# Kernel tuning notes

Hardware: AMD Instinct MI355X
Metric: run time of the kernel (lower is better)

## Reference

```python
import jax, jax.numpy as jnp
import numpy as np

B, C, H, W = 4, 512, 64, 64
CQ = C // 8


def setup_inputs() -> dict:
    key = jax.random.key(0)
    ks = jax.random.split(key, 8)
    s_in = 1.0 / np.sqrt(C)
    return {
        "x": jax.random.normal(ks[0], (B, C, H, W), jnp.float32),
        "wq": jax.random.normal(ks[1], (CQ, C), jnp.float32) * s_in,
        "bq": jax.random.normal(ks[2], (CQ,), jnp.float32) * 0.01,
        "wk": jax.random.normal(ks[3], (CQ, C), jnp.float32) * s_in,
        "bk": jax.random.normal(ks[4], (CQ,), jnp.float32) * 0.01,
        "wv": jax.random.normal(ks[5], (C, C), jnp.float32) * s_in,
        "bv": jax.random.normal(ks[6], (C,), jnp.float32) * 0.01,
        "gamma": jax.random.normal(ks[7], (1,), jnp.float32) * 0.1,
    }


def reference(x, wq, bq, wk, bk, wv, bv, gamma):
    b, c, h, w = x.shape
    n = h * w
    xf = x.reshape(b, c, n)  # [B, C, N]; 1x1 conv == channel matmul
    q = jnp.einsum("oc,bcn->bon", wq, xf) + bq[None, :, None]  # [B, CQ, N]
    k = jnp.einsum("oc,bcn->bon", wk, xf) + bk[None, :, None]  # [B, CQ, N]
    v = jnp.einsum("oc,bcn->bon", wv, xf) + bv[None, :, None]  # [B, C, N]
    energy = jnp.einsum("bcn,bcm->bnm", q, k)  # [B, N, N]
    attn = jax.nn.softmax(energy, axis=-1)
    out = jnp.einsum("bcm,bnm->bcn", v, attn)  # [B, C, N]
    out = out.reshape(b, c, h, w)
    return gamma[0] * out + x
```

## Files before the change

kernel.cpp:

```cpp
#include <hip/hip_runtime.h>
#include <hip/hip_bf16.h>

#define BATCH 4
#define CH    512
#define NPIX  4096
#define LOG2E 1.4426950408889634f

#define BOFF  327680
#define WTOT  328320
#define PSTR  268

typedef float v4f __attribute__((ext_vector_type(4)));
typedef short v8s __attribute__((ext_vector_type(8)));
typedef unsigned short u16;

__device__ __forceinline__ float b2f(u16 v){
    union { unsigned u; float f; } x; x.u = ((unsigned)v) << 16; return x.f;
}
__device__ __forceinline__ u16 f2b(float f){
    union { float f; unsigned u; } x; x.f = f;
    unsigned r = x.u + 0x7fffu + ((x.u >> 16) & 1u);
    return (u16)(r >> 16);
}
__device__ __forceinline__ void f2b2(float a, float b, u16* o){
    union { __hip_bfloat162 v; u16 s[2]; } u;
    u.v = __float22bfloat162_rn(make_float2(a, b));
    o[0] = u.s[0]; o[1] = u.s[1];
}
__device__ __forceinline__ float fexp2(float x){
#if __has_builtin(__builtin_amdgcn_exp2f)
    return __builtin_amdgcn_exp2f(x);
#else
    return exp2f(x);
#endif
}
__device__ __forceinline__ v4f mfma16(v8s a, v8s b, v4f c){
    return __builtin_amdgcn_mfma_f32_16x16x32_bf16(a, b, c, 0, 0, 0);
}
__device__ __forceinline__ float load_s(const void* p, size_t idx, int isf32){
    return isf32 ? ((const float*)p)[idx] : b2f(((const u16*)p)[idx]);
}

__device__ __forceinline__ int sniff_isf32(const unsigned* __restrict__ xw,
                                           int t, int nthr, int* cnt){
    if (t == 0) *cnt = 0;
    __syncthreads();
    int c = 0;
    for (int i = t; i < 1024; i += nthr){
        unsigned e = (xw[i] >> 23) & 0xFFu;
        if (e >= 64u && e < 192u) c++;
    }
    c += __shfl_xor(c, 1);  c += __shfl_xor(c, 2);  c += __shfl_xor(c, 4);
    c += __shfl_xor(c, 8);  c += __shfl_xor(c, 16); c += __shfl_xor(c, 32);
    if ((t & 63) == 0) atomicAdd(cnt, c);
    __syncthreads();
    return (*cnt > 512) ? 1 : 0;
}

__global__ __launch_bounds__(256) void prep_kernel(
    const void* __restrict__ wq, const void* __restrict__ bq,
    const void* __restrict__ wk, const void* __restrict__ bk,
    const void* __restrict__ wv, const void* __restrict__ bv,
    const void* __restrict__ x, u16* __restrict__ wall)
{
    __shared__ int scnt;
    const int isf32 = sniff_isf32((const unsigned*)x, threadIdx.x, 256, &scnt);

    int i = blockIdx.x * 256 + threadIdx.x;
    if (i >= WTOT) return;
    float v;
    if (i < BOFF){
        int o = i >> 9, c = i & 511;
        if (o < 64)       v = load_s(wq, (size_t)o * 512 + c, isf32);
        else if (o < 128) v = load_s(wk, (size_t)(o - 64) * 512 + c, isf32);
        else              v = load_s(wv, (size_t)(o - 128) * 512 + c, isf32);
    } else {
        int o = i - BOFF;
        if (o < 64)       v = load_s(bq, o, isf32);
        else if (o < 128) v = load_s(bk, o - 64, isf32);
        else              v = load_s(bv, o - 128, isf32);
    }
    wall[i] = f2b(v);
}

__global__ __launch_bounds__(256, 3) void proj_kernel(
    const void* __restrict__ x, const u16* __restrict__ wall,
    u16* __restrict__ Qf, u16* __restrict__ Kf, u16* __restrict__ Vf,
    u16* __restrict__ xbf)
{
    __shared__ __align__(16) u16 xT[2][64 * 40];
    __shared__ int scnt;

    const int isf32 = sniff_isf32((const unsigned*)x, threadIdx.x, 256, &scnt);

    const int ntile = blockIdx.x, os = blockIdx.y, b = blockIdx.z;
    const int n0 = ntile * 64;
    const int t = threadIdx.x, lane = t & 63, w = t >> 6, q = lane >> 4, col = lane & 15;

    const int rrow  = t >> 3;
    const int ncol8 = (t & 7) * 8;
    const int xswz  = (t & 3) << 3;
    const size_t xbase = (size_t)b * CH * NPIX + n0 + ncol8;

    v4f acc[5][4];
    #pragma unroll
    for (int i = 0; i < 5; i++)
        #pragma unroll
        for (int j = 0; j < 4; j++) acc[i][j] = (v4f){0.f, 0.f, 0.f, 0.f};

    float4 gn0, gn1;

    #define LOADX(cb_) do {                                                  \
        const size_t src = xbase + (size_t)((cb_) * 32 + rrow) * NPIX;       \
        if (isf32){ gn0 = *(const float4*)((const float*)x + src);           \
                    gn1 = *(const float4*)((const float*)x + src + 4); }     \
        else { union { uint4 v; float4 f; } lu;                              \
               lu.v = *(const uint4*)((const u16*)x + src); gn0 = lu.f; }    \
    } while (0)

    #define CVT8(vals_) do {                                                 \
        if (isf32){ f2b2(gn0.x, gn0.y, &vals_[0]); f2b2(gn0.z, gn0.w, &vals_[2]); \
                    f2b2(gn1.x, gn1.y, &vals_[4]); f2b2(gn1.z, gn1.w, &vals_[6]); } \
        else { union { float4 f; uint4 v; } uu; uu.f = gn0;                  \
               *(uint4*)vals_ = uu.v; }                                      \
    } while (0)

    {
        LOADX(0);
        u16 vals[8]; CVT8(vals);
        #pragma unroll
        for (int i = 0; i < 8; i++) xT[0][(ncol8 + i) * 40 + (rrow ^ xswz)] = vals[i];
        if (os == 0)
            *(uint4*)&xbf[(size_t)(b * CH + rrow) * NPIX + n0 + ncol8] = *(uint4*)vals;
        LOADX(1);
    }
    __syncthreads();

    for (int cb = 0; cb < 16; cb++){
        const int buf = cb & 1;
        const int c0 = cb * 32 + q * 8;

        v8s wf[5];
        #pragma unroll
        for (int ct = 0; ct < 5; ct++)
            wf[ct] = *(const v8s*)&wall[(size_t)(320 * os + 80 * w + 16 * ct + col) * 512 + c0];

        v8s a[4];
        #pragma unroll
        for (int g = 0; g < 4; g++){
            const int rsw = ((2 * g + (col >> 3)) & 3) << 3;
            a[g] = *(const v8s*)&xT[buf][(16 * g + col) * 40 + (rsw ^ (q * 8))];
        }

        if (cb < 15){
            u16 vals[8]; CVT8(vals);
            #pragma unroll
            for (int i = 0; i < 8; i++) xT[buf ^ 1][(ncol8 + i) * 40 + (rrow ^ xswz)] = vals[i];
            if (os == 0)
                *(uint4*)&xbf[(size_t)(b * CH + (cb + 1) * 32 + rrow) * NPIX + n0 + ncol8] = *(uint4*)vals;
            if (cb < 14) LOADX(cb + 2);
        }

        #pragma unroll
        for (int ct = 0; ct < 5; ct++)
            #pragma unroll
            for (int g = 0; g < 4; g++)
                acc[ct][g] = mfma16(a[g], wf[ct], acc[ct][g]);
        __syncthreads();
    }
    #undef LOADX
    #undef CVT8

    const u16* ball = wall + BOFF;
    #pragma unroll
    for (int ct = 0; ct < 5; ct++){
        const int o = 320 * os + 80 * w + 16 * ct + col;
        const float bv_ = b2f(ball[o]);
        #pragma unroll
        for (int g = 0; g < 4; g++){
            const int nb = n0 + 16 * g + 4 * q;
            if (o < 64){
                const int k = o;
                size_t base = (size_t)b * NPIX * 64
                    + ((size_t)((nb >> 4) * 2 + (k >> 5))) * 512
                    + ((k & 31) >> 3) * 128 + (nb & 15) * 8 + (k & 7);
                #pragma unroll
                for (int r = 0; r < 4; r++)
                    Qf[base + r * 8] = f2b((acc[ct][g][r] + bv_) * LOG2E);
            } else if (o < 128){
                const int k = o - 64;
                size_t base = (size_t)b * NPIX * 64
                    + ((size_t)((nb >> 4) * 2 + (k >> 5))) * 512
                    + ((k & 31) >> 3) * 128 + (nb & 15) * 8 + (k & 7);
                #pragma unroll
                for (int r = 0; r < 4; r++)
                    Kf[base + r * 8] = f2b(acc[ct][g][r] + bv_);
            } else {
                const int c = o - 128;
                size_t base = (size_t)b * CH * NPIX
                    + ((size_t)((c >> 4) * 128 + (nb >> 5))) * 512
                    + ((nb & 31) >> 3) * 128 + (c & 15) * 8 + (nb & 7);
                union { uint2 u; u16 s[4]; } ov;
                #pragma unroll
                for (int r = 0; r < 4; r++)
                    ov.s[r] = f2b(acc[ct][g][r] + bv_);
                *(uint2*)&Vf[base] = ov.u;
            }
        }
    }
}

__global__ __launch_bounds__(512, 4) void attn_kernel(
    const void* __restrict__ x,
    const u16* __restrict__ Qf, const u16* __restrict__ Kf, const u16* __restrict__ Vf,
    const u16* __restrict__ xbf, const void* __restrict__ gamma,
    void* __restrict__ out)
{
    __shared__ __align__(16) u16  Plds[2][64 * PSTR];
    __shared__ __align__(16) float lsum[8][64];
    __shared__ int scnt;

    const int isf32 = sniff_isf32((const unsigned*)x, threadIdx.x, 512, &scnt);

    const int bid = blockIdx.x;
    const int csplit = bid & 1;
    const int b      = (bid >> 1) & 3;
    const int ntile  = bid >> 3;
    const int n0 = ntile * 64;

    const int t = threadIdx.x, lane = t & 63, w = t >> 6, q = lane >> 4, col = lane & 15;

    const u16* Qb = Qf + (size_t)b * NPIX * 64;
    const u16* Kb = Kf + (size_t)b * NPIX * 64;
    const u16* Vb = Vf + (size_t)b * CH * NPIX;

    v8s qa[4][2];
    #pragma unroll
    for (int g = 0; g < 4; g++)
        #pragma unroll
        for (int c2 = 0; c2 < 2; c2++)
            qa[g][c2] = *(const v8s*)&Qb[(size_t)(((n0 >> 4) + g) * 2 + c2) * 512 + lane * 8];

    float lreg[4] = {0.f, 0.f, 0.f, 0.f};

    v4f oacc[2][4];
    #pragma unroll
    for (int i = 0; i < 2; i++)
        #pragma unroll
        for (int j = 0; j < 4; j++) oacc[i][j] = (v4f){0.f, 0.f, 0.f, 0.f};

    const int ms    = 32 * w;
    const int cslab = csplit * 256 + 32 * w;

    for (int it = 0; it < 16; it++){
        const int m0 = it * 256;
        const int buf = it & 1;

        v8s kf[2][2];
        #pragma unroll
        for (int mt = 0; mt < 2; mt++)
            #pragma unroll
            for (int c2 = 0; c2 < 2; c2++)
                kf[mt][c2] = *(const v8s*)&Kb[(size_t)((((m0 + ms) >> 4) + mt) * 2 + c2) * 512 + lane * 8];

        #pragma unroll
        for (int g = 0; g < 4; g++){
            #pragma unroll
            for (int mt = 0; mt < 2; mt++){
                v4f sv = (v4f){-64.f, -64.f, -64.f, -64.f};
                sv = mfma16(kf[mt][0], qa[g][0], sv);
                sv = mfma16(kf[mt][1], qa[g][1], sv);
                float p0 = fexp2(sv[0]), p1 = fexp2(sv[1]);
                float p2 = fexp2(sv[2]), p3 = fexp2(sv[3]);
                lreg[g] += (p0 + p1) + (p2 + p3);
                union { uint2 u; u16 s[4]; } pk;
                f2b2(p0, p1, &pk.s[0]);
                f2b2(p2, p3, &pk.s[2]);
                *(uint2*)&Plds[buf][(16 * g + col) * PSTR + ms + 16 * mt + 4 * q] = pk.u;
            }
        }

        __syncthreads();

        v8s va_c[2];
        #pragma unroll
        for (int ct = 0; ct < 2; ct++)
            va_c[ct] = *(const v8s*)&Vb[(size_t)(((cslab + 16 * ct) >> 4) * 128 + (m0 >> 5)) * 512 + lane * 8];
        #pragma unroll
        for (int kk = 0; kk < 8; kk++){
            v8s va_n[2];
            if (kk < 7){
                #pragma unroll
                for (int ct = 0; ct < 2; ct++)
                    va_n[ct] = *(const v8s*)&Vb[(size_t)(((cslab + 16 * ct) >> 4) * 128 + (m0 >> 5) + kk + 1) * 512 + lane * 8];
            }
            v8s pb[4];
            #pragma unroll
            for (int nt = 0; nt < 4; nt++)
                pb[nt] = *(const v8s*)&Plds[buf][(16 * nt + col) * PSTR + 32 * kk + q * 8];
            __builtin_amdgcn_s_setprio(1);
            #pragma unroll
            for (int ct = 0; ct < 2; ct++)
                #pragma unroll
                for (int nt = 0; nt < 4; nt++)
                    oacc[ct][nt] = mfma16(va_c[ct], pb[nt], oacc[ct][nt]);
            __builtin_amdgcn_s_setprio(0);
            #pragma unroll
            for (int ct = 0; ct < 2; ct++) va_c[ct] = va_n[ct];
        }
    }

    #pragma unroll
    for (int g = 0; g < 4; g++){
        lreg[g] += __shfl_xor(lreg[g], 16);
        lreg[g] += __shfl_xor(lreg[g], 32);
    }
    if (lane < 16){
        #pragma unroll
        for (int g = 0; g < 4; g++)
            lsum[w][16 * g + lane] = lreg[g];
    }
    __syncthreads();

    const float gam = load_s(gamma, 0, isf32);
    float linv[4];
    #pragma unroll
    for (int nt = 0; nt < 4; nt++){
        int nn = 16 * nt + col;
        float l = ((lsum[0][nn] + lsum[1][nn]) + (lsum[2][nn] + lsum[3][nn]))
                + ((lsum[4][nn] + lsum[5][nn]) + (lsum[6][nn] + lsum[7][nn]));
        linv[nt] = gam / l;
    }

    const size_t boff = (size_t)b * CH * NPIX;
    #pragma unroll
    for (int ct = 0; ct < 2; ct++){
        #pragma unroll
        for (int rr = 0; rr < 4; rr++){
            int c = cslab + 16 * ct + 4 * q + rr;
            size_t base = boff + (size_t)c * NPIX + n0;
            #pragma unroll
            for (int nt = 0; nt < 4; nt++){
                int n = 16 * nt + col;
                float o = oacc[ct][nt][rr] * linv[nt] + b2f(xbf[base + n]);
                if (isf32) ((float*)out)[base + n] = o;
                else       ((u16*)out)[base + n]  = f2b(o);
            }
        }
    }
}

extern "C" void kernel_launch(void* const* d_in, const int* in_sizes, int n_in,
                              void* d_out, int out_size, void* d_ws, size_t ws_size,
                              hipStream_t stream)
{
    const void* x     = d_in[0];
    const void* wq    = d_in[1];
    const void* bq    = d_in[2];
    const void* wk    = d_in[3];
    const void* bk    = d_in[4];
    const void* wv    = d_in[5];
    const void* bv    = d_in[6];
    const void* gamma = d_in[7];

    u16* Qf   = (u16*)d_ws;
    u16* Kf   = Qf + (size_t)1048576;
    u16* Vf   = Kf + (size_t)1048576;
    u16* xbf  = Vf + (size_t)8388608;
    u16* wall = xbf + (size_t)8388608;

    prep_kernel<<<(WTOT + 255) / 256, 256, 0, stream>>>(wq, bq, wk, bk, wv, bv, x, wall);
    proj_kernel<<<dim3(64, 2, BATCH), 256, 0, stream>>>(x, wall, Qf, Kf, Vf, xbf);
    attn_kernel<<<512, 512, 0, stream>>>(x, Qf, Kf, Vf, xbf, gamma, d_out);
}
```

Measured before the change: 207.6 us.

## Stage two channel blocks per barrier and pre-tile weights for coalesced fragment loads

The projection kernel now processes two 32-channel blocks per iteration. LDS tiles are doubled and two global x loads are kept in flight, which halves the number of __syncthreads. The prep kernel writes the weight matrix in a tiled order so each warp's MFMA B-fragments for a block are contiguous 512-element chunks, replacing strided row reads. Occupancy hint drops from 3 to 2 blocks per CU to make room for the extra registers and LDS.

```diff
diff --git a/kernel.cpp b/kernel.cpp
--- a/kernel.cpp
+++ b/kernel.cpp
@@ -74,21 +74,27 @@
         if (o < 64)       v = load_s(wq, (size_t)o * 512 + c, isf32);
         else if (o < 128) v = load_s(wk, (size_t)(o - 64) * 512 + c, isf32);
         else              v = load_s(wv, (size_t)(o - 128) * 512 + c, isf32);
+        const int os = o / 320, rem = o % 320;
+        const int w = rem / 80, ct = (rem % 80) / 16, col = rem % 16;
+        const int cb = c >> 5, q = (c >> 3) & 3, e = c & 7;
+        const size_t idx = (size_t)(((os * 4 + w) * 5 + ct) * 16 + cb) * 512
+                         + col * 32 + q * 8 + e;
+        wall[idx] = f2b(v);
     } else {
         int o = i - BOFF;
         if (o < 64)       v = load_s(bq, o, isf32);
         else if (o < 128) v = load_s(bk, o - 64, isf32);
         else              v = load_s(bv, o - 128, isf32);
-    }
-    wall[i] = f2b(v);
-}
-
-__global__ __launch_bounds__(256, 3) void proj_kernel(
+        wall[i] = f2b(v);
+    }
+}
+
+__global__ __launch_bounds__(256, 2) void proj_kernel(
     const void* __restrict__ x, const u16* __restrict__ wall,
     u16* __restrict__ Qf, u16* __restrict__ Kf, u16* __restrict__ Vf,
     u16* __restrict__ xbf)
 {
-    __shared__ __align__(16) u16 xT[2][64 * 40];
+    __shared__ __align__(16) u16 xT[2][64 * 80];
     __shared__ int scnt;
 
     const int isf32 = sniff_isf32((const unsigned*)x, threadIdx.x, 256, &scnt);
@@ -101,6 +107,7 @@
     const int ncol8 = (t & 7) * 8;
     const int xswz  = (t & 3) << 3;
     const size_t xbase = (size_t)b * CH * NPIX + n0 + ncol8;
+    const int wof   = (os * 4 + w) * 80;
 
     v4f acc[5][4];
     #pragma unroll
@@ -108,68 +115,97 @@
         #pragma unroll
         for (int j = 0; j < 4; j++) acc[i][j] = (v4f){0.f, 0.f, 0.f, 0.f};
 
-    float4 gn0, gn1;
-
-    #define LOADX(cb_) do {                                                  \
+    float4 gA0, gA1, gB0, gB1;
+
+    #define LOADX(cb_, g0_, g1_) do {                                        \
         const size_t src = xbase + (size_t)((cb_) * 32 + rrow) * NPIX;       \
-        if (isf32){ gn0 = *(const float4*)((const float*)x + src);           \
-                    gn1 = *(const float4*)((const float*)x + src + 4); }     \
+        if (isf32){ g0_ = *(const float4*)((const float*)x + src);           \
+                    g1_ = *(const float4*)((const float*)x + src + 4); }     \
         else { union { uint4 v; float4 f; } lu;                              \
-               lu.v = *(const uint4*)((const u16*)x + src); gn0 = lu.f; }    \
+               lu.v = *(const uint4*)((const u16*)x + src); g0_ = lu.f; }    \
     } while (0)
 
-    #define CVT8(vals_) do {                                                 \
-        if (isf32){ f2b2(gn0.x, gn0.y, &vals_[0]); f2b2(gn0.z, gn0.w, &vals_[2]); \
-                    f2b2(gn1.x, gn1.y, &vals_[4]); f2b2(gn1.z, gn1.w, &vals_[6]); } \
-        else { union { float4 f; uint4 v; } uu; uu.f = gn0;                  \
+    #define CVT8(vals_, g0_, g1_) do {                                       \
+        if (isf32){ f2b2(g0_.x, g0_.y, &vals_[0]); f2b2(g0_.z, g0_.w, &vals_[2]); \
+                    f2b2(g1_.x, g1_.y, &vals_[4]); f2b2(g1_.z, g1_.w, &vals_[6]); } \
+        else { union { float4 f; uint4 v; } uu; uu.f = g0_;                  \
                *(uint4*)vals_ = uu.v; }                                      \
     } while (0)
 
+    #define STAGE(cb_, buf_, ch_, g0_, g1_) do {                             \
+        u16 vals[8]; CVT8(vals, g0_, g1_);                                   \
+        _Pragma("unroll")                                                    \
+        for (int i = 0; i < 8; i++)                                          \
+            xT[buf_][(ncol8 + i) * 80 + (ch_) * 40 + (rrow ^ xswz)] = vals[i]; \
+        if (os == 0)                                                         \
+            *(uint4*)&xbf[(size_t)(b * CH + (cb_) * 32 + rrow) * NPIX + n0 + ncol8] = *(uint4*)vals; \
+    } while (0)
+
     {
-        LOADX(0);
-        u16 vals[8]; CVT8(vals);
-        #pragma unroll
-        for (int i = 0; i < 8; i++) xT[0][(ncol8 + i) * 40 + (rrow ^ xswz)] = vals[i];
-        if (os == 0)
-            *(uint4*)&xbf[(size_t)(b * CH + rrow) * NPIX + n0 + ncol8] = *(uint4*)vals;
-        LOADX(1);
+        LOADX(0, gA0, gA1);
+        STAGE(0, 0, 0, gA0, gA1);
+        LOADX(1, gB0, gB1);
+        STAGE(1, 0, 1, gB0, gB1);
+        LOADX(2, gA0, gA1);
+        LOADX(3, gB0, gB1);
     }
     __syncthreads();
 
-    for (int cb = 0; cb < 16; cb++){
-        const int buf = cb & 1;
-        const int c0 = cb * 32 + q * 8;
-
-        v8s wf[5];
-        #pragma unroll
-        for (int ct = 0; ct < 5; ct++)
-            wf[ct] = *(const v8s*)&wall[(size_t)(320 * os + 80 * w + 16 * ct + col) * 512 + c0];
-
-        v8s a[4];
-        #pragma unroll
-        for (int g = 0; g < 4; g++){
-            const int rsw = ((2 * g + (col >> 3)) & 3) << 3;
-            a[g] = *(const v8s*)&xT[buf][(16 * g + col) * 40 + (rsw ^ (q * 8))];
-        }
-
-        if (cb < 15){
-            u16 vals[8]; CVT8(vals);
-            #pragma unroll
-            for (int i = 0; i < 8; i++) xT[buf ^ 1][(ncol8 + i) * 40 + (rrow ^ xswz)] = vals[i];
-            if (os == 0)
-                *(uint4*)&xbf[(size_t)(b * CH + (cb + 1) * 32 + rrow) * NPIX + n0 + ncol8] = *(uint4*)vals;
-            if (cb < 14) LOADX(cb + 2);
-        }
-
-        #pragma unroll
-        for (int ct = 0; ct < 5; ct++)
-            #pragma unroll
-            for (int g = 0; g < 4; g++)
-                acc[ct][g] = mfma16(a[g], wf[ct], acc[ct][g]);
+    for (int p = 0; p < 8; p++){
+        const int buf = p & 1;
+
+        {
+            const int cb = 2 * p;
+            v8s wf[5];
+            #pragma unroll
+            for (int ct = 0; ct < 5; ct++)
+                wf[ct] = *(const v8s*)&wall[(size_t)(wof + ct * 16 + cb) * 512 + col * 32 + q * 8];
+            v8s a[4];
+            #pragma unroll
+            for (int g = 0; g < 4; g++){
+                const int rsw = ((2 * g + (col >> 3)) & 3) << 3;
+                a[g] = *(const v8s*)&xT[buf][(16 * g + col) * 80 + (rsw ^ (q * 8))];
+            }
+            #pragma unroll
+            for (int ct = 0; ct < 5; ct++)
+                #pragma unroll
+                for (int g = 0; g < 4; g++)
+                    acc[ct][g] = mfma16(a[g], wf[ct], acc[ct][g]);
+        }
+
+        if (p < 7){
+            STAGE(2 * p + 2, buf ^ 1, 0, gA0, gA1);
+            STAGE(2 * p + 3, buf ^ 1, 1, gB0, gB1);
+        }
+
+        {
+            const int cb = 2 * p + 1;
+            v8s wf[5];
+            #pragma unroll
+            for (int ct = 0; ct < 5; ct++)
+                wf[ct] = *(const v8s*)&wall[(size_t)(wof + ct * 16 + cb) * 512 + col * 32 + q * 8];
+            v8s a[4];
+            #pragma unroll
+            for (int g = 0; g < 4; g++){
+                const int rsw = ((2 * g + (col >> 3)) & 3) << 3;
+                a[g] = *(const v8s*)&xT[buf][(16 * g + col) * 80 + 40 + (rsw ^ (q * 8))];
+            }
+            #pragma unroll
+            for (int ct = 0; ct < 5; ct++)
+                #pragma unroll
+                for (int g = 0; g < 4; g++)
+                    acc[ct][g] = mfma16(a[g], wf[ct], acc[ct][g]);
+        }
+
+        if (p < 6){
+            LOADX(2 * p + 4, gA0, gA1);
+            LOADX(2 * p + 5, gB0, gB1);
+        }
         __syncthreads();
     }
     #undef LOADX
     #undef CVT8
+    #undef STAGE
 
     const u16* ball = wall + BOFF;
     #pragma unroll
```

After: 205.8 us, median of 3. About the same (-0.9%).
